# Kernel tuning notes

Hardware: AMD Instinct MI355X
Metric: run time of the kernel (lower is better)

Reference implementation:

```python
import jax, jax.numpy as jnp
import numpy as np

N, E, F_IN, HID, OUT, B = 8192, 262144, 128, 256, 128, 64


def setup_inputs() -> dict:
    key = jax.random.key(0)
    ks = jax.random.split(key, 8)
    node_features = jax.random.normal(ks[0], (N, F_IN), dtype=jnp.float32)
    edge_index = jax.random.randint(ks[1], (2, E), 0, N, dtype=jnp.int64)
    batch = jnp.sort(jax.random.randint(ks[2], (N,), 0, B, dtype=jnp.int64))
    # GCN layer params (nn.Linear: y = x @ W + b)
    W1 = jax.random.normal(ks[3], (F_IN, HID), dtype=jnp.float32) / np.sqrt(F_IN)
    b1 = jax.random.normal(ks[4], (HID,), dtype=jnp.float32) * 0.01
    W2 = jax.random.normal(ks[5], (HID, OUT), dtype=jnp.float32) / np.sqrt(HID)
    b2 = jax.random.normal(ks[6], (OUT,), dtype=jnp.float32) * 0.01
    return {
        "node_features": node_features,
        "W1": W1, "b1": b1, "W2": W2, "b2": b2,
        "edge_index": edge_index,
        "batch": batch,
        "num_graphs": B,
    }


def _normalized_adjacency(edge_index, num_nodes, dtype):
    src, dst = edge_index[0], edge_index[1]
    A = jnp.zeros((num_nodes, num_nodes), dtype=dtype)
    A = A.at[src, dst].set(1.0).at[dst, src].set(1.0)  # undirected, set (dedups)
    A = A + jnp.eye(num_nodes, dtype=dtype)            # self-loops
    deg = A.sum(axis=1)
    dis = jnp.where(deg > 0, jax.lax.rsqrt(jnp.where(deg > 0, deg, 1.0)), 0.0)
    return dis[:, None] * A * dis[None, :]


def reference(node_features, W1, b1, W2, b2, edge_index, batch, num_graphs):
    n = node_features.shape[0]
    adj = _normalized_adjacency(edge_index, n, node_features.dtype)
    h = jax.nn.relu(adj @ (node_features @ W1 + b1))  # (N, HID)
    h = adj @ (h @ W2 + b2)                            # (N, OUT)
    # mean pooling per graph
    summed = jax.ops.segment_sum(h, batch, num_segments=num_graphs)
    counts = jax.ops.segment_sum(jnp.ones((n,), h.dtype), batch, num_segments=num_graphs)
    return summed / jnp.maximum(counts, 1.0)[:, None]
```

## Files before the change

kernel.cpp:

```cpp
#include <hip/hip_runtime.h>
#include <hip/hip_bf16.h>

#define N_NODES 8192
#define N_EDGES 262144
#define F_INDIM 128
#define HID 256
#define F_OUT 128
#define N_GRAPHS 64
#define WPR (N_NODES / 32)
#define CAP 160
#define NQ 32

struct alignas(8) bf4 { __hip_bfloat16 a, b, c, d; };

__device__ inline float2 bf2unpack(unsigned int u) {
    float2 r;
    r.x = __uint_as_float(u << 16);
    r.y = __uint_as_float(u & 0xffff0000u);
    return r;
}

__global__ __launch_bounds__(256) void cast_x(const float* __restrict__ X,
                                              __hip_bfloat16* __restrict__ Xh) {
    int i = blockIdx.x * 256 + threadIdx.x;
    float4 v = ((const float4*)X)[i];
    bf4 o;
    o.a = __float2bfloat16(v.x); o.b = __float2bfloat16(v.y);
    o.c = __float2bfloat16(v.z); o.d = __float2bfloat16(v.w);
    ((bf4*)Xh)[i] = o;
}

__global__ __launch_bounds__(256) void scatter_edges(const int* __restrict__ ei,
                                                     unsigned int* __restrict__ mask) {
    int e = blockIdx.x * blockDim.x + threadIdx.x;
    if (e >= N_EDGES) return;
    int s = ei[e];
    int d = ei[N_EDGES + e];
    if ((unsigned)s >= N_NODES || (unsigned)d >= N_NODES) return;
    atomicOr(&mask[(size_t)s * WPR + (d >> 5)], 1u << (d & 31));
    atomicOr(&mask[(size_t)d * WPR + (s >> 5)], 1u << (s & 31));
}

__global__ __launch_bounds__(256) void build_adj(const unsigned int* __restrict__ mask,
                                                 int* __restrict__ adj,
                                                 int* __restrict__ deg,
                                                 float* __restrict__ dis) {
    int row = (blockIdx.x * blockDim.x + threadIdx.x) >> 6;
    int lane = threadIdx.x & 63;
    if (row >= N_NODES) return;
    const uint4* r = (const uint4*)(mask + (size_t)row * WPR);
    uint4 v = r[lane];
    int cnt = __popc(v.x) + __popc(v.y) + __popc(v.z) + __popc(v.w);
    int scan = cnt;
    for (int off = 1; off < 64; off <<= 1) {
        int n = __shfl_up(scan, off);
        if (lane >= off) scan += n;
    }
    int tot = __shfl(scan, 63);
    int idx = scan - cnt;
    int* ap = adj + (size_t)row * CAP;
    int wbase = lane << 7;
    unsigned int wd;
    wd = v.x; while (wd) { int b = __ffs(wd) - 1; wd &= wd - 1; if (idx < CAP) ap[idx] = wbase + b;      ++idx; }
    wd = v.y; while (wd) { int b = __ffs(wd) - 1; wd &= wd - 1; if (idx < CAP) ap[idx] = wbase + 32 + b; ++idx; }
    wd = v.z; while (wd) { int b = __ffs(wd) - 1; wd &= wd - 1; if (idx < CAP) ap[idx] = wbase + 64 + b; ++idx; }
    wd = v.w; while (wd) { int b = __ffs(wd) - 1; wd &= wd - 1; if (idx < CAP) ap[idx] = wbase + 96 + b; ++idx; }
    if (lane == 63) { deg[row] = tot; dis[row] = rsqrtf((float)(tot + 1)); }
}

__global__ __launch_bounds__(256) void spmm_x_fused(const int* __restrict__ adj,
                                                    const int* __restrict__ deg,
                                                    const __hip_bfloat16* __restrict__ Xh,
                                                    const float* __restrict__ dis,
                                                    const int* __restrict__ batch,
                                                    float* __restrict__ G,
                                                    float* __restrict__ sv,
                                                    float* __restrict__ u) {
    int w = threadIdx.x >> 6, lane = threadIdx.x & 63;
    int i = blockIdx.x * 4 + w;
    __shared__ int nb[4][CAP];
    __shared__ float nbd[4][CAP];
    __shared__ float ul[4][64];
    int d = deg[i]; if (d > CAP) d = CAP;
    const unsigned int* Xu = (const unsigned int*)Xh;
    ul[w][lane] = 0.0f;
    float p = 0.0f;
    for (int t = lane; t < d; t += 64) {
        int j = adj[(size_t)i * CAP + t];
        float dj = dis[j];
        nb[w][t] = j; nbd[w][t] = dj;
        p += dj;
    }
    __syncthreads();
    for (int t = lane; t < d; t += 64)
        atomicAdd(&ul[w][batch[nb[w][t]] & 63], nbd[w][t]);
    for (int off = 32; off; off >>= 1) p += __shfl_down(p, off);
    float di = dis[i];
    if (lane == 0) {
        sv[i] = di * (di + p);
        atomicAdd(&ul[w][batch[i] & 63], di);
    }
    float2 xi = bf2unpack(Xu[(size_t)i * 64 + lane]);
    float2 a0 = {di * xi.x, di * xi.y};
    float2 a1 = {0,0}, a2 = {0,0}, a3 = {0,0}, a4 = {0,0}, a5 = {0,0}, a6 = {0,0}, a7 = {0,0};
    int k = 0;
    for (; k + 8 <= d; k += 8) {
#define GATH(Q, ACC) { int j = nb[w][k+Q]; float dj = nbd[w][k+Q]; \
        float2 f = bf2unpack(Xu[(size_t)j * 64 + lane]); \
        ACC.x += dj * f.x; ACC.y += dj * f.y; }
        GATH(0, a0) GATH(1, a1) GATH(2, a2) GATH(3, a3)
        GATH(4, a4) GATH(5, a5) GATH(6, a6) GATH(7, a7)
    }
    for (; k < d; ++k) GATH(0, a0)
#undef GATH
    float2 s;
    s.x = ((a0.x + a1.x) + (a2.x + a3.x)) + ((a4.x + a5.x) + (a6.x + a7.x));
    s.y = ((a0.y + a1.y) + (a2.y + a3.y)) + ((a4.y + a5.y) + (a6.y + a7.y));
    float2 o = {di * s.x, di * s.y};
    ((float2*)(G + (size_t)i * F_INDIM))[lane] = o;
    __syncthreads();
    u[(size_t)i * N_GRAPHS + lane] = ul[w][lane];
}

__global__ __launch_bounds__(256) void fused_gemm(const float* __restrict__ G,
                                                  const float* __restrict__ W1,
                                                  const float* __restrict__ b1,
                                                  const float* __restrict__ sv,
                                                  const float* __restrict__ W2,
                                                  const float* __restrict__ b2,
                                                  const float* __restrict__ dis,
                                                  __hip_bfloat16* __restrict__ M2ph) {
    int i0 = blockIdx.x * 16;
    int t = threadIdx.x;
    __shared__ float xs[16][F_INDIM];
    __shared__ float hs[16][HID];
    for (int v = t; v < 16 * F_INDIM / 4; v += 256) {
        int r = v >> 5, c4 = (v & 31) << 2;
        *(float4*)&xs[r][c4] = *(const float4*)&G[(size_t)(i0 + r) * F_INDIM + c4];
    }
    __syncthreads();
    {
        int tc = t & 63, tr = t >> 6;
        float4 acc0 = {0,0,0,0}, acc1 = {0,0,0,0}, acc2 = {0,0,0,0}, acc3 = {0,0,0,0};
        const float* wp = W1 + 4 * tc;
        for (int k = 0; k < F_INDIM; k += 4) {
            float4 w0 = *(const float4*)&wp[(size_t)(k + 0) * HID];
            float4 w1 = *(const float4*)&wp[(size_t)(k + 1) * HID];
            float4 w2 = *(const float4*)&wp[(size_t)(k + 2) * HID];
            float4 w3 = *(const float4*)&wp[(size_t)(k + 3) * HID];
#define ROW(R, ACC) { \
            float4 g4 = *(const float4*)&xs[4 * tr + R][k]; \
            ACC.x += g4.x*w0.x; ACC.y += g4.x*w0.y; ACC.z += g4.x*w0.z; ACC.w += g4.x*w0.w; \
            ACC.x += g4.y*w1.x; ACC.y += g4.y*w1.y; ACC.z += g4.y*w1.z; ACC.w += g4.y*w1.w; \
            ACC.x += g4.z*w2.x; ACC.y += g4.z*w2.y; ACC.z += g4.z*w2.z; ACC.w += g4.z*w2.w; \
            ACC.x += g4.w*w3.x; ACC.y += g4.w*w3.y; ACC.z += g4.w*w3.z; ACC.w += g4.w*w3.w; }
            ROW(0, acc0) ROW(1, acc1) ROW(2, acc2) ROW(3, acc3)
#undef ROW
        }
        float4 b = *(const float4*)&b1[4 * tc];
#define EPI(R, ACC) { \
            int r = 4 * tr + R; float s = sv[i0 + r]; float4 res = ACC; \
            hs[r][4 * tc + 0] = fmaxf(res.x + s * b.x, 0.f); \
            hs[r][4 * tc + 1] = fmaxf(res.y + s * b.y, 0.f); \
            hs[r][4 * tc + 2] = fmaxf(res.z + s * b.z, 0.f); \
            hs[r][4 * tc + 3] = fmaxf(res.w + s * b.w, 0.f); }
        EPI(0, acc0) EPI(1, acc1) EPI(2, acc2) EPI(3, acc3)
#undef EPI
    }
    __syncthreads();
    {
        int tc = t & 31, tr = t >> 5;
        float4 acc0 = {0,0,0,0}, acc1 = {0,0,0,0};
        const float* wp = W2 + 4 * tc;
        for (int k = 0; k < HID; k += 4) {
            float4 w0 = *(const float4*)&wp[(size_t)(k + 0) * F_OUT];
            float4 w1 = *(const float4*)&wp[(size_t)(k + 1) * F_OUT];
            float4 w2 = *(const float4*)&wp[(size_t)(k + 2) * F_OUT];
            float4 w3 = *(const float4*)&wp[(size_t)(k + 3) * F_OUT];
#define ROW(R, ACC) { \
            float4 g4 = *(const float4*)&hs[2 * tr + R][k]; \
            ACC.x += g4.x*w0.x; ACC.y += g4.x*w0.y; ACC.z += g4.x*w0.z; ACC.w += g4.x*w0.w; \
            ACC.x += g4.y*w1.x; ACC.y += g4.y*w1.y; ACC.z += g4.y*w1.z; ACC.w += g4.y*w1.w; \
            ACC.x += g4.z*w2.x; ACC.y += g4.z*w2.y; ACC.z += g4.z*w2.z; ACC.w += g4.z*w2.w; \
            ACC.x += g4.w*w3.x; ACC.y += g4.w*w3.y; ACC.z += g4.w*w3.z; ACC.w += g4.w*w3.w; }
            ROW(0, acc0) ROW(1, acc1)
#undef ROW
        }
        float4 b = *(const float4*)&b2[4 * tc];
#define EPI(R, ACC) { \
            int i = i0 + 2 * tr + R; float dd = dis[i]; float4 res = ACC; \
            bf4 o; o.a = __float2bfloat16(dd * (res.x + b.x)); o.b = __float2bfloat16(dd * (res.y + b.y)); \
            o.c = __float2bfloat16(dd * (res.z + b.z)); o.d = __float2bfloat16(dd * (res.w + b.w)); \
            *(bf4*)(M2ph + (size_t)i * F_OUT + 4 * tc) = o; }
        EPI(0, acc0) EPI(1, acc1)
#undef EPI
    }
}

__global__ __launch_bounds__(128) void wpool_a(const float* __restrict__ u,
                                               const __hip_bfloat16* __restrict__ M2ph,
                                               float* __restrict__ part) {
    int g = blockIdx.x, q = blockIdx.y, c = threadIdx.x;
    int j0 = q * (N_NODES / NQ);
    const unsigned short* Mu = (const unsigned short*)M2ph;
    __shared__ float us[N_NODES / NQ];
    us[c]       = u[(size_t)(j0 + c) * N_GRAPHS + g];
    us[c + 128] = u[(size_t)(j0 + c + 128) * N_GRAPHS + g];
    __syncthreads();
    float a0 = 0.f, a1 = 0.f, a2 = 0.f, a3 = 0.f, a4 = 0.f, a5 = 0.f, a6 = 0.f, a7 = 0.f;
    for (int jj = 0; jj < N_NODES / NQ; jj += 8) {
#define TERM(Q, ACC) ACC += us[jj + Q] * __uint_as_float((unsigned)Mu[(size_t)(j0 + jj + Q) * F_OUT + c] << 16);
        TERM(0, a0) TERM(1, a1) TERM(2, a2) TERM(3, a3)
        TERM(4, a4) TERM(5, a5) TERM(6, a6) TERM(7, a7)
#undef TERM
    }
    float s = ((a0 + a1) + (a2 + a3)) + ((a4 + a5) + (a6 + a7));
    part[((size_t)g * NQ + q) * F_OUT + c] = s;
}

__global__ __launch_bounds__(128) void wpool_b(const float* __restrict__ part,
                                               const int* __restrict__ batch,
                                               float* __restrict__ out) {
    int g = blockIdx.x, c = threadIdx.x;
    int lo = 0, hi = N_NODES;
    while (lo < hi) { int m = (lo + hi) >> 1; if (batch[m] < g) lo = m + 1; else hi = m; }
    int start = lo;
    hi = N_NODES;
    while (lo < hi) { int m = (lo + hi) >> 1; if (batch[m] < g + 1) lo = m + 1; else hi = m; }
    int cnt = lo - start;
    float s = 0.0f;
#pragma unroll
    for (int q = 0; q < NQ; ++q) s += part[((size_t)g * NQ + q) * F_OUT + c];
    out[(size_t)g * F_OUT + c] = s / (float)(cnt > 0 ? cnt : 1);
}

extern "C" void kernel_launch(void* const* d_in, const int* in_sizes, int n_in,
                              void* d_out, int out_size, void* d_ws, size_t ws_size,
                              hipStream_t stream) {
    const float* X  = (const float*)d_in[0];
    const float* W1 = (const float*)d_in[1];
    const float* b1 = (const float*)d_in[2];
    const float* W2 = (const float*)d_in[3];
    const float* b2 = (const float*)d_in[4];
    const int* ei    = (const int*)d_in[5];
    const int* batch = (const int*)d_in[6];
    float* out = (float*)d_out;

    char* ws = (char*)d_ws;
    unsigned int* mask   = (unsigned int*)(ws);
    float* u             = (float*)(ws);
    __hip_bfloat16* M2ph = (__hip_bfloat16*)(ws + 2097152);
    float* part          = (float*)(ws + 4194304);
    float* G   = (float*)(ws + 8388608);
    __hip_bfloat16* Xh = (__hip_bfloat16*)(ws + 12582912);
    int*   adj = (int*)(ws + 25165824);
    int*   deg = (int*)(ws + 30408704);
    float* dis = (float*)(ws + 30441472);
    float* sv  = (float*)(ws + 30474240);

    cast_x<<<(N_NODES * F_INDIM / 4) / 256, 256, 0, stream>>>(X, Xh);
    hipMemsetAsync(mask, 0, (size_t)N_NODES * WPR * sizeof(unsigned int), stream);
    scatter_edges<<<N_EDGES / 256, 256, 0, stream>>>(ei, mask);
    build_adj<<<N_NODES / 4, 256, 0, stream>>>(mask, adj, deg, dis);
    spmm_x_fused<<<N_NODES / 4, 256, 0, stream>>>(adj, deg, Xh, dis, batch, G, sv, u);
    fused_gemm<<<N_NODES / 16, 256, 0, stream>>>(G, W1, b1, sv, W2, b2, dis, M2ph);
    wpool_a<<<dim3(N_GRAPHS, NQ), 128, 0, stream>>>(u, M2ph, part);
    wpool_b<<<N_GRAPHS, 128, 0, stream>>>(part, batch, out);
}
```

Measured before the change: 161.4 us.

## Fuse mask zeroing into cast, scan bitmask in SpMM, atomically reduce pooling

The memset of the adjacency bitmask is folded into the bf16 cast kernel as extra blocks. The CSR-like adjacency list buffer is removed. Degrees are computed in a light popcount kernel, and the SpMM kernel rebuilds each row's neighbor list from the bitmask directly in shared memory, avoiding a global write and read of the list. The two-stage pooling reduction becomes one kernel using atomicAdd into the output, which the GEMM kernel zeroes first. Together this cuts the launch count and intermediate traffic, at the cost of reading the mask twice and making the final sums order-nondeterministic.

```diff
diff --git a/kernel.cpp b/kernel.cpp
--- a/kernel.cpp
+++ b/kernel.cpp
@@ -20,14 +20,22 @@
     return r;
 }
 
-__global__ __launch_bounds__(256) void cast_x(const float* __restrict__ X,
-                                              __hip_bfloat16* __restrict__ Xh) {
-    int i = blockIdx.x * 256 + threadIdx.x;
-    float4 v = ((const float4*)X)[i];
-    bf4 o;
-    o.a = __float2bfloat16(v.x); o.b = __float2bfloat16(v.y);
-    o.c = __float2bfloat16(v.z); o.d = __float2bfloat16(v.w);
-    ((bf4*)Xh)[i] = o;
+__global__ __launch_bounds__(256) void cast_zero(const float* __restrict__ X,
+                                                 __hip_bfloat16* __restrict__ Xh,
+                                                 unsigned int* __restrict__ mask) {
+    int b = blockIdx.x, t = threadIdx.x;
+    if (b < 1024) {
+        int i = b * 256 + t;
+        float4 v = ((const float4*)X)[i];
+        bf4 o;
+        o.a = __float2bfloat16(v.x); o.b = __float2bfloat16(v.y);
+        o.c = __float2bfloat16(v.z); o.d = __float2bfloat16(v.w);
+        ((bf4*)Xh)[i] = o;
+    } else {
+        int i = (b - 1024) * 256 + t;
+        uint4 z = {0u, 0u, 0u, 0u};
+        ((uint4*)mask)[i] = z;
+    }
 }
 
 __global__ __launch_bounds__(256) void scatter_edges(const int* __restrict__ ei,
@@ -41,15 +49,30 @@
     atomicOr(&mask[(size_t)d * WPR + (s >> 5)], 1u << (s & 31));
 }
 
-__global__ __launch_bounds__(256) void build_adj(const unsigned int* __restrict__ mask,
-                                                 int* __restrict__ adj,
-                                                 int* __restrict__ deg,
-                                                 float* __restrict__ dis) {
+__global__ __launch_bounds__(256) void compute_dis(const unsigned int* __restrict__ mask,
+                                                   float* __restrict__ dis) {
     int row = (blockIdx.x * blockDim.x + threadIdx.x) >> 6;
     int lane = threadIdx.x & 63;
-    if (row >= N_NODES) return;
-    const uint4* r = (const uint4*)(mask + (size_t)row * WPR);
-    uint4 v = r[lane];
+    uint4 v = ((const uint4*)(mask + (size_t)row * WPR))[lane];
+    int c = __popc(v.x) + __popc(v.y) + __popc(v.z) + __popc(v.w);
+    for (int off = 32; off; off >>= 1) c += __shfl_down(c, off);
+    if (lane == 0) dis[row] = rsqrtf((float)(c + 1));
+}
+
+__global__ __launch_bounds__(256) void spmm_scan(const unsigned int* __restrict__ mask,
+                                                 const __hip_bfloat16* __restrict__ Xh,
+                                                 const float* __restrict__ dis,
+                                                 const int* __restrict__ batch,
+                                                 float* __restrict__ G,
+                                                 float* __restrict__ sv,
+                                                 float* __restrict__ u) {
+    int w = threadIdx.x >> 6, lane = threadIdx.x & 63;
+    int i = blockIdx.x * 4 + w;
+    __shared__ int nb[4][CAP];
+    __shared__ float nbd[4][CAP];
+    __shared__ float ul[4][64];
+    ul[w][lane] = 0.0f;
+    uint4 v = ((const uint4*)(mask + (size_t)i * WPR))[lane];
     int cnt = __popc(v.x) + __popc(v.y) + __popc(v.z) + __popc(v.w);
     int scan = cnt;
     for (int off = 1; off < 64; off <<= 1) {
@@ -58,48 +81,30 @@
     }
     int tot = __shfl(scan, 63);
     int idx = scan - cnt;
-    int* ap = adj + (size_t)row * CAP;
     int wbase = lane << 7;
     unsigned int wd;
-    wd = v.x; while (wd) { int b = __ffs(wd) - 1; wd &= wd - 1; if (idx < CAP) ap[idx] = wbase + b;      ++idx; }
-    wd = v.y; while (wd) { int b = __ffs(wd) - 1; wd &= wd - 1; if (idx < CAP) ap[idx] = wbase + 32 + b; ++idx; }
-    wd = v.z; while (wd) { int b = __ffs(wd) - 1; wd &= wd - 1; if (idx < CAP) ap[idx] = wbase + 64 + b; ++idx; }
-    wd = v.w; while (wd) { int b = __ffs(wd) - 1; wd &= wd - 1; if (idx < CAP) ap[idx] = wbase + 96 + b; ++idx; }
-    if (lane == 63) { deg[row] = tot; dis[row] = rsqrtf((float)(tot + 1)); }
-}
-
-__global__ __launch_bounds__(256) void spmm_x_fused(const int* __restrict__ adj,
-                                                    const int* __restrict__ deg,
-                                                    const __hip_bfloat16* __restrict__ Xh,
-                                                    const float* __restrict__ dis,
-                                                    const int* __restrict__ batch,
-                                                    float* __restrict__ G,
-                                                    float* __restrict__ sv,
-                                                    float* __restrict__ u) {
-    int w = threadIdx.x >> 6, lane = threadIdx.x & 63;
-    int i = blockIdx.x * 4 + w;
-    __shared__ int nb[4][CAP];
-    __shared__ float nbd[4][CAP];
-    __shared__ float ul[4][64];
-    int d = deg[i]; if (d > CAP) d = CAP;
+    wd = v.x; while (wd) { int b = __ffs(wd) - 1; wd &= wd - 1; if (idx < CAP) nb[w][idx] = wbase + b;      ++idx; }
+    wd = v.y; while (wd) { int b = __ffs(wd) - 1; wd &= wd - 1; if (idx < CAP) nb[w][idx] = wbase + 32 + b; ++idx; }
+    wd = v.z; while (wd) { int b = __ffs(wd) - 1; wd &= wd - 1; if (idx < CAP) nb[w][idx] = wbase + 64 + b; ++idx; }
+    wd = v.w; while (wd) { int b = __ffs(wd) - 1; wd &= wd - 1; if (idx < CAP) nb[w][idx] = wbase + 96 + b; ++idx; }
+    int d = tot; if (d > CAP) d = CAP;
+    __syncthreads();
     const unsigned int* Xu = (const unsigned int*)Xh;
-    ul[w][lane] = 0.0f;
     float p = 0.0f;
     for (int t = lane; t < d; t += 64) {
-        int j = adj[(size_t)i * CAP + t];
+        int j = nb[w][t];
         float dj = dis[j];
-        nb[w][t] = j; nbd[w][t] = dj;
+        nbd[w][t] = dj;
         p += dj;
-    }
-    __syncthreads();
-    for (int t = lane; t < d; t += 64)
-        atomicAdd(&ul[w][batch[nb[w][t]] & 63], nbd[w][t]);
+        atomicAdd(&ul[w][batch[j] & 63], dj);
+    }
     for (int off = 32; off; off >>= 1) p += __shfl_down(p, off);
     float di = dis[i];
     if (lane == 0) {
         sv[i] = di * (di + p);
         atomicAdd(&ul[w][batch[i] & 63], di);
     }
+    __syncthreads();
     float2 xi = bf2unpack(Xu[(size_t)i * 64 + lane]);
     float2 a0 = {di * xi.x, di * xi.y};
     float2 a1 = {0,0}, a2 = {0,0}, a3 = {0,0}, a4 = {0,0}, a5 = {0,0}, a6 = {0,0}, a7 = {0,0};
@@ -118,7 +123,6 @@
     s.y = ((a0.y + a1.y) + (a2.y + a3.y)) + ((a4.y + a5.y) + (a6.y + a7.y));
     float2 o = {di * s.x, di * s.y};
     ((float2*)(G + (size_t)i * F_INDIM))[lane] = o;
-    __syncthreads();
     u[(size_t)i * N_GRAPHS + lane] = ul[w][lane];
 }
 
@@ -129,9 +133,14 @@
                                                   const float* __restrict__ W2,
                                                   const float* __restrict__ b2,
                                                   const float* __restrict__ dis,
-                                                  __hip_bfloat16* __restrict__ M2ph) {
+                                                  __hip_bfloat16* __restrict__ M2ph,
+                                                  float* __restrict__ out) {
     int i0 = blockIdx.x * 16;
     int t = threadIdx.x;
+    if (blockIdx.x == 0) {
+        float4 z = {0,0,0,0};
+        for (int v = t; v < N_GRAPHS * F_OUT / 4; v += 256) ((float4*)out)[v] = z;
+    }
     __shared__ float xs[16][F_INDIM];
     __shared__ float hs[16][HID];
     for (int v = t; v < 16 * F_INDIM / 4; v += 256) {
@@ -197,9 +206,10 @@
     }
 }
 
-__global__ __launch_bounds__(128) void wpool_a(const float* __restrict__ u,
-                                               const __hip_bfloat16* __restrict__ M2ph,
-                                               float* __restrict__ part) {
+__global__ __launch_bounds__(128) void wpool(const float* __restrict__ u,
+                                             const __hip_bfloat16* __restrict__ M2ph,
+                                             const int* __restrict__ batch,
+                                             float* __restrict__ out) {
     int g = blockIdx.x, q = blockIdx.y, c = threadIdx.x;
     int j0 = q * (N_NODES / NQ);
     const unsigned short* Mu = (const unsigned short*)M2ph;
@@ -215,23 +225,13 @@
 #undef TERM
     }
     float s = ((a0 + a1) + (a2 + a3)) + ((a4 + a5) + (a6 + a7));
-    part[((size_t)g * NQ + q) * F_OUT + c] = s;
-}
-
-__global__ __launch_bounds__(128) void wpool_b(const float* __restrict__ part,
-                                               const int* __restrict__ batch,
-                                               float* __restrict__ out) {
-    int g = blockIdx.x, c = threadIdx.x;
     int lo = 0, hi = N_NODES;
     while (lo < hi) { int m = (lo + hi) >> 1; if (batch[m] < g) lo = m + 1; else hi = m; }
     int start = lo;
     hi = N_NODES;
     while (lo < hi) { int m = (lo + hi) >> 1; if (batch[m] < g + 1) lo = m + 1; else hi = m; }
     int cnt = lo - start;
-    float s = 0.0f;
-#pragma unroll
-    for (int q = 0; q < NQ; ++q) s += part[((size_t)g * NQ + q) * F_OUT + c];
-    out[(size_t)g * F_OUT + c] = s / (float)(cnt > 0 ? cnt : 1);
+    atomicAdd(&out[(size_t)g * F_OUT + c], s / (float)(cnt > 0 ? cnt : 1));
 }
 
 extern "C" void kernel_launch(void* const* d_in, const int* in_sizes, int n_in,
@@ -248,22 +248,17 @@
 
     char* ws = (char*)d_ws;
     unsigned int* mask   = (unsigned int*)(ws);
-    float* u             = (float*)(ws);
     __hip_bfloat16* M2ph = (__hip_bfloat16*)(ws + 2097152);
-    float* part          = (float*)(ws + 4194304);
     float* G   = (float*)(ws + 8388608);
     __hip_bfloat16* Xh = (__hip_bfloat16*)(ws + 12582912);
-    int*   adj = (int*)(ws + 25165824);
-    int*   deg = (int*)(ws + 30408704);
+    float* u   = (float*)(ws + 14680064);
     float* dis = (float*)(ws + 30441472);
     float* sv  = (float*)(ws + 30474240);
 
-    cast_x<<<(N_NODES * F_INDIM / 4) / 256, 256, 0, stream>>>(X, Xh);
-    hipMemsetAsync(mask, 0, (size_t)N_NODES * WPR * sizeof(unsigned int), stream);
+    cast_zero<<<3072, 256, 0, stream>>>(X, Xh, mask);
     scatter_edges<<<N_EDGES / 256, 256, 0, stream>>>(ei, mask);
-    build_adj<<<N_NODES / 4, 256, 0, stream>>>(mask, adj, deg, dis);
-    spmm_x_fused<<<N_NODES / 4, 256, 0, stream>>>(adj, deg, Xh, dis, batch, G, sv, u);
-    fused_gemm<<<N_NODES / 16, 256, 0, stream>>>(G, W1, b1, sv, W2, b2, dis, M2ph);
-    wpool_a<<<dim3(N_GRAPHS, NQ), 128, 0, stream>>>(u, M2ph, part);
-    wpool_b<<<N_GRAPHS, 128, 0, stream>>>(part, batch, out);
-}
+    compute_dis<<<N_NODES / 4, 256, 0, stream>>>(mask, dis);
+    spmm_scan<<<N_NODES / 4, 256, 0, stream>>>(mask, Xh, dis, batch, G, sv, u);
+    fused_gemm<<<N_NODES / 16, 256, 0, stream>>>(G, W1, b1, sv, W2, b2, dis, M2ph, out);
+    wpool<<<dim3(N_GRAPHS, NQ), 128, 0, stream>>>(u, M2ph, batch, out);
+}
```

After: 154.4 us. 1.05x faster.
